# Kernel optimization log

Hardware: AMD Instinct MI355X
Metric: run time of the kernel (lower is better)

The kernel has to match this reference:

```python
import jax, jax.numpy as jnp
from jax import lax
import numpy as np

EPS = 1e-6
B, CIN, HW = 16, 12, 40
E, DEPTH, NH = 768, 12, 12
K, PAD = 10, 5
S = (HW + 2 * PAD - K) // 1 + 1  # 41 (series_len = s0); s1 also 41
L = S * S
HD = E // NH
MLP = 4 * E


def _ln(x, w, b):
    mu = x.mean(-1, keepdims=True)
    xc = x - mu
    var = (xc * xc).mean(-1, keepdims=True)
    return xc * lax.rsqrt(var + EPS) * w + b


def setup_inputs() -> dict:
    key = jax.random.key(0)
    ks = iter(jax.random.split(key, 24))
    r = lambda shape, s=0.02: jax.random.normal(next(ks), shape, jnp.float32) * s
    inp = {
        'x': jax.random.normal(next(ks), (B, CIN, HW, HW), jnp.float32),
        'conv_w': r((E, CIN, K, K)), 'conv_b': jnp.zeros((E,), jnp.float32),
        'pos_embed': r((1, L, E)),
        'ln1_w': jnp.ones((DEPTH, E), jnp.float32), 'ln1_b': jnp.zeros((DEPTH, E), jnp.float32),
        'qkv_w': r((DEPTH, E, 3 * E)), 'qkv_b': jnp.zeros((DEPTH, 3 * E), jnp.float32),
        'proj_w': r((DEPTH, E, E)), 'proj_b': jnp.zeros((DEPTH, E), jnp.float32),
        'ln2_w': jnp.ones((DEPTH, E), jnp.float32), 'ln2_b': jnp.zeros((DEPTH, E), jnp.float32),
        'fc1_w': r((DEPTH, E, MLP)), 'fc1_b': jnp.zeros((DEPTH, MLP), jnp.float32),
        'fc2_w': r((DEPTH, MLP, E)), 'fc2_b': jnp.zeros((DEPTH, E), jnp.float32),
        'lnf_w': jnp.ones((E,), jnp.float32), 'lnf_b': jnp.zeros((E,), jnp.float32),
        'tconv_w': r((E, 1, K, K)), 'tconv_b': jnp.zeros((1,), jnp.float32),
    }
    return inp


def reference(x, conv_w, conv_b, pos_embed, ln1_w, ln1_b, qkv_w, qkv_b,
              proj_w, proj_b, ln2_w, ln2_b, fc1_w, fc1_b, fc2_w, fc2_b,
              lnf_w, lnf_b, tconv_w, tconv_b):
    scale = HD ** -0.5
    # patch embed: Conv2d -> (B, E, 41, 41) -> flatten -> (B, L, E)
    h = lax.conv_general_dilated(x, conv_w, (1, 1), [(PAD, PAD), (PAD, PAD)])
    h = h + conv_b[None, :, None, None]
    t = h.reshape(B, E, L).transpose(0, 2, 1) + pos_embed

    for i in range(DEPTH):
        # attention over each of the S series slices (N = S tokens each), batched
        y = _ln(t, ln1_w[i], ln1_b[i])
        qkv = (y @ qkv_w[i] + qkv_b[i]).reshape(B, S, S, 3, NH, HD)
        q, k, v = qkv[:, :, :, 0], qkv[:, :, :, 1], qkv[:, :, :, 2]  # (B,S,N,NH,HD)
        attn = jnp.einsum('bsnhd,bsmhd->bshnm', q, k) * scale
        attn = jax.nn.softmax(attn, axis=-1)
        o = jnp.einsum('bshnm,bsmhd->bsnhd', attn, v).reshape(B, L, E)
        t = t + (o @ proj_w[i] + proj_b[i])
        # MLP
        z = _ln(t, ln2_w[i], ln2_b[i])
        z = jax.nn.gelu(z @ fc1_w[i] + fc1_b[i], approximate=False)
        t = t + (z @ fc2_w[i] + fc2_b[i])

    t = _ln(t, lnf_w, lnf_b)
    feat = t.reshape(B, S, S, E).transpose(0, 3, 1, 2)  # (B, E, 41, 41)
    # ConvTranspose2d(k=10, s=1, p=5) == direct conv with flipped/swapped kernel, pad k-1-p=4
    wt = jnp.flip(tconv_w, (2, 3)).transpose(1, 0, 2, 3)  # (out_c, E, K, K)
    out = lax.conv_general_dilated(feat, wt, (1, 1), [(K - 1 - PAD,) * 2] * 2)
    out = out + tconv_b[None, :, None, None]
    return jnp.squeeze(out)  # (B, 40, 40)
```

## Files before the change

kernel.cpp:

```cpp
#include <hip/hip_runtime.h>
#include <cstdint>

typedef __bf16 bf16_t;
typedef __attribute__((ext_vector_type(8))) __bf16 bf16x8;
typedef __attribute__((ext_vector_type(4))) __bf16 bf16x4;
typedef __attribute__((ext_vector_type(4))) float f32x4;

#define TOKENS 26896
#define LLEN   1681
#define SDIM   41
#define EDIM   768

__device__ __forceinline__ void gload_lds16(const bf16_t* g, bf16_t* l) {
  auto gp = reinterpret_cast<const __attribute__((address_space(1))) char*>(
      reinterpret_cast<uintptr_t>(g));
  auto lp = reinterpret_cast<__attribute__((address_space(3))) char*>(
      reinterpret_cast<uintptr_t>(l));
  __builtin_amdgcn_global_load_lds(gp, lp, 16, 0, 0);
}

enum { EPI_T_POS = 0, EPI_BF16 = 1, EPI_ADD_T = 2, EPI_GELU = 3, EPI_F32 = 4 };

template <int EPI>
__global__ __launch_bounds__(256, 3) void gemm4_kernel(
    const bf16_t* __restrict__ A, const bf16_t* __restrict__ Bt,
    const float* __restrict__ bias, float* __restrict__ fout,
    bf16_t* __restrict__ bout, const float* __restrict__ pos,
    int M, int N, int K, int ntn, int nwg, int mtiles)
{
  __shared__ bf16_t lds[3 * 8192];
  const int tid = threadIdx.x, wave = tid >> 6, lane = tid & 63;
  const int wr = wave >> 1, wc = wave & 1;

  int id = blockIdx.x;
  {
    const int q = nwg >> 3, r = nwg & 7;
    const int xcd = id & 7, ix = id >> 3;
    id = (xcd < r ? xcd * (q + 1) : r * (q + 1) + (xcd - r) * q) + ix;
  }
  const int gsz = mtiles * 6;
  const int cg  = id / gsz, rem = id % gsz;
  const int row0 = (rem / 6) * 128;
  const int col0 = (cg * 6 + rem % 6) * 128;
  const int NT = K >> 5;

  const int srow = tid >> 2;
  const int sswz = ((tid & 3) ^ ((srow >> 1) & 3)) * 8;
  const bf16_t* aptr[2];
  const bf16_t* bptr[2];
  #pragma unroll
  for (int p = 0; p < 2; ++p) {
    int ar = row0 + p * 64 + srow; if (ar > M - 1) ar = M - 1;
    int br = col0 + p * 64 + srow; if (br > N - 1) br = N - 1;
    aptr[p] = A  + (size_t)ar * K + sswz;
    bptr[p] = Bt + (size_t)br * K + sswz;
  }
  bf16_t* sdst = lds + tid * 8;

  #define STAGE(BUF, KT) do {                                   \
    const int koff_ = (KT) << 5;                                \
    gload_lds16(aptr[0] + koff_, sdst + (BUF)*8192);            \
    gload_lds16(aptr[1] + koff_, sdst + (BUF)*8192 + 2048);     \
    gload_lds16(bptr[0] + koff_, sdst + (BUF)*8192 + 4096);     \
    gload_lds16(bptr[1] + koff_, sdst + (BUF)*8192 + 6144);     \
  } while (0)

  const int l15 = lane & 15, l4 = lane >> 4;
  const int fswz = (l4 ^ ((l15 >> 1) & 3)) << 3;
  const bf16_t* lA = lds + (wr * 64 + l15) * 32 + fswz;
  const bf16_t* lB = lds + 4096 + (wc * 64 + l15) * 32 + fswz;

  f32x4 acc[4][4] = {};

  #define COMPUTE(BUF) do {                                     \
    bf16x8 fa[4], fb[4];                                        \
    _Pragma("unroll")                                           \
    for (int m_ = 0; m_ < 4; ++m_) fa[m_] = *(const bf16x8*)(lA + (BUF)*8192 + m_*512); \
    _Pragma("unroll")                                           \
    for (int n_ = 0; n_ < 4; ++n_) fb[n_] = *(const bf16x8*)(lB + (BUF)*8192 + n_*512); \
    _Pragma("unroll")                                           \
    for (int m_ = 0; m_ < 4; ++m_)                              \
      _Pragma("unroll")                                         \
      for (int n_ = 0; n_ < 4; ++n_)                            \
        acc[m_][n_] = __builtin_amdgcn_mfma_f32_16x16x32_bf16(fa[m_], fb[n_], acc[m_][n_], 0, 0, 0); \
  } while (0)

  #define STEP(SC, SN, T) do {                                  \
    if ((T) + 2 < NT) STAGE(SN, (T) + 2);                       \
    COMPUTE(SC);                                                \
    if ((T) + 2 < NT)      asm volatile("s_waitcnt vmcnt(4)" ::: "memory"); \
    else if ((T) + 1 < NT) asm volatile("s_waitcnt vmcnt(0)" ::: "memory"); \
    __builtin_amdgcn_s_barrier();                               \
    __builtin_amdgcn_sched_barrier(0);                          \
  } while (0)

  STAGE(0, 0);
  if (NT > 1) {
    STAGE(1, 1);
    asm volatile("s_waitcnt vmcnt(4)" ::: "memory");
  } else {
    asm volatile("s_waitcnt vmcnt(0)" ::: "memory");
  }
  __builtin_amdgcn_s_barrier();
  __builtin_amdgcn_sched_barrier(0);

  for (int kt = 0; kt < NT; kt += 3) {
    STEP(0, 2, kt);
    if (kt + 1 < NT) STEP(1, 0, kt + 1);
    if (kt + 2 < NT) STEP(2, 1, kt + 2);
  }
  #undef STEP
  #undef STAGE
  #undef COMPUTE

  const int rgrp = lane >> 4;
  #pragma unroll
  for (int m = 0; m < 4; ++m) {
    #pragma unroll
    for (int n = 0; n < 4; ++n) {
      const int col = col0 + wc * 64 + n * 16 + l15;
      if (col >= N) continue;
      const int rbase = row0 + wr * 64 + m * 16 + rgrp * 4;
      float bv = 0.f;
      if constexpr (EPI != EPI_F32) bv = bias[col];
      #pragma unroll
      for (int r = 0; r < 4; ++r) {
        const int rr = rbase + r;
        if (rr >= M) continue;
        const float v = acc[m][n][r] + bv;
        const size_t o = (size_t)rr * N + col;
        if constexpr (EPI == EPI_T_POS) {
          const int l = rr % LLEN;
          bout[o] = (bf16_t)(v + pos[(size_t)l * N + col]);
        } else if constexpr (EPI == EPI_BF16) {
          bout[o] = (bf16_t)v;
        } else if constexpr (EPI == EPI_ADD_T) {
          bout[o] = (bf16_t)((float)bout[o] + v);
        } else if constexpr (EPI == EPI_GELU) {
          const float u = v + 0.044715f * v * v * v;
          const float gg = v / (1.f + __expf(-1.5957691216f * u));
          bout[o] = (bf16_t)gg;
        } else {
          fout[o] = v;
        }
      }
    }
  }
}

__global__ __launch_bounds__(256) void gemm128_f32(
    const bf16_t* __restrict__ A, const bf16_t* __restrict__ Bt,
    float* __restrict__ fout, int M, int N, int K)
{
  __shared__ bf16_t As[128 * 32];
  __shared__ bf16_t Bs[128 * 32];
  const int tid = threadIdx.x, wave = tid >> 6, lane = tid & 63;
  const int row0 = blockIdx.x * 128, col0 = blockIdx.y * 128;
  const int wr = wave >> 1, wc = wave & 1;
  f32x4 acc[4][4] = {};
  const int srow = lane >> 2, skoff = (lane & 3) * 8;
  const int nsteps = K >> 5;
  for (int kt = 0; kt < nsteps; ++kt) {
    const int k0 = kt << 5;
    #pragma unroll
    for (int i = 0; i < 2; ++i) {
      const int r = (i * 4 + wave) * 16 + srow;
      int arow = row0 + r; if (arow > M - 1) arow = M - 1;
      int brow = col0 + r; if (brow > N - 1) brow = N - 1;
      gload_lds16(A  + (size_t)arow * K + k0 + skoff, &As[r * 32 + skoff]);
      gload_lds16(Bt + (size_t)brow * K + k0 + skoff, &Bs[r * 32 + skoff]);
    }
    asm volatile("s_waitcnt vmcnt(0)" ::: "memory");
    __syncthreads();
    const int lrow = lane & 15, lk = (lane >> 4) * 8;
    bf16x8 af[4], bfr[4];
    #pragma unroll
    for (int mi = 0; mi < 4; ++mi)
      af[mi] = *(const bf16x8*)&As[(wr * 64 + mi * 16 + lrow) * 32 + lk];
    #pragma unroll
    for (int ni = 0; ni < 4; ++ni)
      bfr[ni] = *(const bf16x8*)&Bs[(wc * 64 + ni * 16 + lrow) * 32 + lk];
    #pragma unroll
    for (int mi = 0; mi < 4; ++mi)
      #pragma unroll
      for (int ni = 0; ni < 4; ++ni)
        acc[mi][ni] = __builtin_amdgcn_mfma_f32_16x16x32_bf16(af[mi], bfr[ni], acc[mi][ni], 0, 0, 0);
    __syncthreads();
  }
  const int lcol = lane & 15, rgrp = lane >> 4;
  #pragma unroll
  for (int mi = 0; mi < 4; ++mi)
    #pragma unroll
    for (int ni = 0; ni < 4; ++ni) {
      const int col = col0 + wc * 64 + ni * 16 + lcol;
      if (col >= N) continue;
      const int rbase = row0 + wr * 64 + mi * 16 + rgrp * 4;
      #pragma unroll
      for (int r = 0; r < 4; ++r) {
        const int rr = rbase + r;
        if (rr >= M) continue;
        fout[(size_t)rr * N + col] = acc[mi][ni][r];
      }
    }
}

__global__ __launch_bounds__(256) void ln_kernel(
    const bf16_t* __restrict__ t, const float* __restrict__ w,
    const float* __restrict__ b, bf16_t* __restrict__ y)
{
  const int token = blockIdx.x * 4 + (threadIdx.x >> 6);
  const int lane  = threadIdx.x & 63;
  const bf16_t* xp = t + (size_t)token * EDIM;
  const bf16x8 a8 = *(const bf16x8*)(xp + lane * 8);
  const bf16x4 a4 = *(const bf16x4*)(xp + 512 + lane * 4);
  float va[12];
  #pragma unroll
  for (int j = 0; j < 8; ++j) va[j] = (float)a8[j];
  #pragma unroll
  for (int j = 0; j < 4; ++j) va[8 + j] = (float)a4[j];
  float s = 0.f;
  #pragma unroll
  for (int j = 0; j < 12; ++j) s += va[j];
  #pragma unroll
  for (int off = 32; off; off >>= 1) s += __shfl_xor(s, off);
  const float mu = s * (1.f / 768.f);
  float q = 0.f;
  #pragma unroll
  for (int j = 0; j < 12; ++j) { const float d = va[j] - mu; q += d * d; }
  #pragma unroll
  for (int off = 32; off; off >>= 1) q += __shfl_xor(q, off);
  const float rs = rsqrtf(q * (1.f / 768.f) + 1e-6f);

  bf16_t* yp = y + (size_t)token * EDIM;
  {
    const int e0 = lane * 8;
    const float4 w0 = ((const float4*)(w + e0))[0];
    const float4 w1 = ((const float4*)(w + e0))[1];
    const float4 b0 = ((const float4*)(b + e0))[0];
    const float4 b1 = ((const float4*)(b + e0))[1];
    bf16x8 o;
    o[0] = (bf16_t)((va[0] - mu) * rs * w0.x + b0.x);
    o[1] = (bf16_t)((va[1] - mu) * rs * w0.y + b0.y);
    o[2] = (bf16_t)((va[2] - mu) * rs * w0.z + b0.z);
    o[3] = (bf16_t)((va[3] - mu) * rs * w0.w + b0.w);
    o[4] = (bf16_t)((va[4] - mu) * rs * w1.x + b1.x);
    o[5] = (bf16_t)((va[5] - mu) * rs * w1.y + b1.y);
    o[6] = (bf16_t)((va[6] - mu) * rs * w1.z + b1.z);
    o[7] = (bf16_t)((va[7] - mu) * rs * w1.w + b1.w);
    *(bf16x8*)(yp + e0) = o;
  }
  {
    const int e0 = 512 + lane * 4;
    const float4 w0 = *(const float4*)(w + e0);
    const float4 b0 = *(const float4*)(b + e0);
    bf16x4 o;
    o[0] = (bf16_t)((va[8]  - mu) * rs * w0.x + b0.x);
    o[1] = (bf16_t)((va[9]  - mu) * rs * w0.y + b0.y);
    o[2] = (bf16_t)((va[10] - mu) * rs * w0.z + b0.z);
    o[3] = (bf16_t)((va[11] - mu) * rs * w0.w + b0.w);
    *(bf16x4*)(yp + e0) = o;
  }
}

__global__ __launch_bounds__(256) void attn_kernel(
    const bf16_t* __restrict__ qkv, bf16_t* __restrict__ o)
{
  const int blk = blockIdx.x;
  const int h  = blk % 12;
  const int bs = blk / 12;
  const int s1 = bs % SDIM;
  const int b  = bs / SDIM;
  __shared__ float Qs[SDIM][68], Ks[SDIM][68], Vs[SDIM][68], Ps[SDIM][44];
  const int tid = threadIdx.x;
  const size_t base = ((size_t)b * LLEN + (size_t)s1 * SDIM);

  for (int idx = tid; idx < SDIM * 8; idx += 256) {
    const int m = idx >> 3, c = idx & 7;
    const bf16_t* p = qkv + (base + m) * 2304 + h * 64 + c * 8;
    const bf16x8 qv = *(const bf16x8*)(p);
    const bf16x8 kv = *(const bf16x8*)(p + 768);
    const bf16x8 vv = *(const bf16x8*)(p + 1536);
    float4 f0, f1;
    f0.x = (float)qv[0]; f0.y = (float)qv[1]; f0.z = (float)qv[2]; f0.w = (float)qv[3];
    f1.x = (float)qv[4]; f1.y = (float)qv[5]; f1.z = (float)qv[6]; f1.w = (float)qv[7];
    *(float4*)&Qs[m][c * 8] = f0; *(float4*)&Qs[m][c * 8 + 4] = f1;
    f0.x = (float)kv[0]; f0.y = (float)kv[1]; f0.z = (float)kv[2]; f0.w = (float)kv[3];
    f1.x = (float)kv[4]; f1.y = (float)kv[5]; f1.z = (float)kv[6]; f1.w = (float)kv[7];
    *(float4*)&Ks[m][c * 8] = f0; *(float4*)&Ks[m][c * 8 + 4] = f1;
    f0.x = (float)vv[0]; f0.y = (float)vv[1]; f0.z = (float)vv[2]; f0.w = (float)vv[3];
    f1.x = (float)vv[4]; f1.y = (float)vv[5]; f1.z = (float)vv[6]; f1.w = (float)vv[7];
    *(float4*)&Vs[m][c * 8] = f0; *(float4*)&Vs[m][c * 8 + 4] = f1;
  }
  __syncthreads();

  for (int idx = tid; idx < SDIM * SDIM; idx += 256) {
    const int n = idx / SDIM, m = idx % SDIM;
    const float4* qn = (const float4*)&Qs[n][0];
    const float4* km = (const float4*)&Ks[m][0];
    float sx = 0.f, sy = 0.f, sz = 0.f, sw = 0.f;
    #pragma unroll
    for (int d4 = 0; d4 < 16; ++d4) {
      const float4 q = qn[d4], k = km[d4];
      sx += q.x * k.x; sy += q.y * k.y; sz += q.z * k.z; sw += q.w * k.w;
    }
    Ps[n][m] = (sx + sy + sz + sw) * 0.125f;
  }
  __syncthreads();

  {
    const int row = tid >> 2, sub = tid & 3;
    if (row < SDIM) {
      float mx = -1e30f;
      for (int m = sub; m < SDIM; m += 4) mx = fmaxf(mx, Ps[row][m]);
      mx = fmaxf(mx, __shfl_xor(mx, 1));
      mx = fmaxf(mx, __shfl_xor(mx, 2));
      float sum = 0.f;
      for (int m = sub; m < SDIM; m += 4) {
        const float e = __expf(Ps[row][m] - mx);
        Ps[row][m] = e;
        sum += e;
      }
      sum += __shfl_xor(sum, 1);
      sum += __shfl_xor(sum, 2);
      const float inv = 1.f / sum;
      for (int m = sub; m < SDIM; m += 4) Ps[row][m] *= inv;
    }
  }
  __syncthreads();

  for (int idx = tid; idx < SDIM * 16; idx += 256) {
    const int n = idx >> 4, dq = idx & 15;
    float ax = 0.f, ay = 0.f, az = 0.f, aw = 0.f;
    #pragma unroll
    for (int m = 0; m < SDIM; ++m) {
      const float pm = Ps[n][m];
      const float4 v = *(const float4*)&Vs[m][dq * 4];
      ax += pm * v.x; ay += pm * v.y; az += pm * v.z; aw += pm * v.w;
    }
    bf16x4 ov;
    ov[0] = (bf16_t)ax; ov[1] = (bf16_t)ay; ov[2] = (bf16_t)az; ov[3] = (bf16_t)aw;
    *(bf16x4*)(o + (base + n) * EDIM + h * 64 + dq * 4) = ov;
  }
}

__device__ __forceinline__ void tr_tile(
    const float* __restrict__ in, bf16_t* __restrict__ out,
    int K, int N, int tile, int tid)
{
  __shared__ float tls[32][33];
  const int ntn = N >> 5;
  const int k0 = (tile / ntn) * 32, n0 = (tile % ntn) * 32;
  const int tx = tid & 31, ty = tid >> 5;
  #pragma unroll
  for (int i = 0; i < 32; i += 8)
    tls[ty + i][tx] = in[(size_t)(k0 + ty + i) * N + n0 + tx];
  __syncthreads();
  #pragma unroll
  for (int i = 0; i < 32; i += 8)
    out[(size_t)(n0 + ty + i) * K + k0 + tx] = (bf16_t)tls[tx][ty + i];
}

__global__ __launch_bounds__(256) void transpose4_kernel(
    const float* __restrict__ qw, const float* __restrict__ pw,
    const float* __restrict__ f1, const float* __restrict__ f2,
    bf16_t* __restrict__ Wq, bf16_t* __restrict__ Wp,
    bf16_t* __restrict__ W1, bf16_t* __restrict__ W2)
{
  const int b = blockIdx.x, tid = threadIdx.x;
  if (b < 1728)       tr_tile(qw, Wq, 768, 2304, b, tid);
  else if (b < 2304)  tr_tile(pw, Wp, 768, 768, b - 1728, tid);
  else if (b < 4608)  tr_tile(f1, W1, 768, 3072, b - 2304, tid);
  else                tr_tile(f2, W2, 3072, 768, b - 4608, tid);
}

__global__ __launch_bounds__(256) void im2col_kernel(
    const float* __restrict__ x, bf16_t* __restrict__ col, int tok0, int ntok)
{
  const size_t idx = (size_t)blockIdx.x * 256 + threadIdx.x;
  if (idx >= (size_t)ntok * 1216) return;
  const int kk = (int)(idx % 1216);
  const size_t tok = tok0 + idx / 1216;
  const int b = (int)(tok / LLEN), l = (int)(tok % LLEN);
  const int s1 = l / SDIM, s2 = l % SDIM;
  float v = 0.f;
  if (kk < 1200) {
    const int cin = kk / 100, r = kk % 100, ky = r / 10, kx = r % 10;
    const int iy = s1 - 5 + ky, ix = s2 - 5 + kx;
    if (iy >= 0 && iy < 40 && ix >= 0 && ix < 40)
      v = x[((size_t)(b * 12 + cin) * 40 + iy) * 40 + ix];
  }
  col[idx] = (bf16_t)v;
}

__global__ __launch_bounds__(256) void convw_kernel(
    const float* __restrict__ w, bf16_t* __restrict__ out)
{
  const int idx = blockIdx.x * 256 + threadIdx.x;
  const int kk = idx % 1216, e = idx / 1216;
  const float v = (kk < 1200) ? w[(size_t)e * 1200 + kk] : 0.f;
  out[idx] = (bf16_t)v;
}

__global__ __launch_bounds__(256) void tconvw_kernel(
    const float* __restrict__ w, bf16_t* __restrict__ out)
{
  const int idx = blockIdx.x * 256 + threadIdx.x;
  const int e = idx % 768, tap = idx / 768;
  const int ky = tap / 10, kx = tap % 10;
  out[idx] = (bf16_t)w[(size_t)e * 100 + (9 - ky) * 10 + (9 - kx)];
}

__global__ __launch_bounds__(256) void outconv_kernel(
    const float* __restrict__ g, const float* __restrict__ tb,
    float* __restrict__ out)
{
  const int idx = blockIdx.x * 256 + threadIdx.x;
  if (idx >= 16 * 40 * 40) return;
  const int x = idx % 40, y = (idx / 40) % 40, b = idx / 1600;
  float s = tb[0];
  #pragma unroll
  for (int ky = 0; ky < 10; ++ky) {
    const int ty_ = y - 4 + ky;
    if (ty_ < 0 || ty_ >= SDIM) continue;
    #pragma unroll
    for (int kx = 0; kx < 10; ++kx) {
      const int tx_ = x - 4 + kx;
      if (tx_ < 0 || tx_ >= SDIM) continue;
      s += g[((size_t)b * LLEN + ty_ * SDIM + tx_) * 100 + ky * 10 + kx];
    }
  }
  out[idx] = s;
}

extern "C" void kernel_launch(void* const* d_in, const int* in_sizes, int n_in,
                              void* d_out, int out_size, void* d_ws, size_t ws_size,
                              hipStream_t stream)
{
  const float* x       = (const float*)d_in[0];
  const float* conv_w  = (const float*)d_in[1];
  const float* conv_b  = (const float*)d_in[2];
  const float* pos     = (const float*)d_in[3];
  const float* ln1_w   = (const float*)d_in[4];
  const float* ln1_b   = (const float*)d_in[5];
  const float* qkv_w   = (const float*)d_in[6];
  const float* qkv_b   = (const float*)d_in[7];
  const float* proj_w  = (const float*)d_in[8];
  const float* proj_b  = (const float*)d_in[9];
  const float* ln2_w   = (const float*)d_in[10];
  const float* ln2_b   = (const float*)d_in[11];
  const float* fc1_w   = (const float*)d_in[12];
  const float* fc1_b   = (const float*)d_in[13];
  const float* fc2_w   = (const float*)d_in[14];
  const float* fc2_b   = (const float*)d_in[15];
  const float* lnf_w   = (const float*)d_in[16];
  const float* lnf_b   = (const float*)d_in[17];
  const float* tconv_w = (const float*)d_in[18];
  const float* tconv_b = (const float*)d_in[19];
  float* out = (float*)d_out;

  const int nch = (ws_size >= 262200000UL) ? 1
                : (ws_size >= 179500000UL) ? 2 : 4;
  const int cht = TOKENS / nch;

  char* p = (char*)d_ws;
  auto alloc = [&](size_t bytes) {
    char* r = p;
    p += (bytes + 255) & ~(size_t)255;
    return r;
  };
  bf16_t* wbuf = (bf16_t*)alloc((size_t)768 * 9216 * 2);
  bf16_t* t    = (bf16_t*)alloc((size_t)TOKENS * EDIM * 2);
  bf16_t* ybuf = (bf16_t*)alloc((size_t)TOKENS * EDIM * 2);
  bf16_t* hbuf = (bf16_t*)alloc((size_t)cht * 3072 * 2);

  bf16_t* Wq = wbuf;
  bf16_t* Wp = Wq + (size_t)2304 * 768;
  bf16_t* W1 = Wp + (size_t)768 * 768;
  bf16_t* W2 = W1 + (size_t)3072 * 768;

  auto g4 = [&](int epi, const bf16_t* A, const bf16_t* Bt,
                const float* bias, bf16_t* bo, const float* pe,
                int M, int N, int K) {
    const int mtiles = (M + 127) / 128;
    const int ntn = N / 128;
    const int nwg = mtiles * ntn;
    switch (epi) {
      case EPI_T_POS: gemm4_kernel<EPI_T_POS><<<nwg, 256, 0, stream>>>(A, Bt, bias, nullptr, bo, pe, M, N, K, ntn, nwg, mtiles); break;
      case EPI_BF16:  gemm4_kernel<EPI_BF16 ><<<nwg, 256, 0, stream>>>(A, Bt, bias, nullptr, bo, pe, M, N, K, ntn, nwg, mtiles); break;
      case EPI_ADD_T: gemm4_kernel<EPI_ADD_T><<<nwg, 256, 0, stream>>>(A, Bt, bias, nullptr, bo, pe, M, N, K, ntn, nwg, mtiles); break;
      default:        gemm4_kernel<EPI_GELU ><<<nwg, 256, 0, stream>>>(A, Bt, bias, nullptr, bo, pe, M, N, K, ntn, nwg, mtiles); break;
    }
  };

  convw_kernel<<<(768 * 1216) / 256, 256, 0, stream>>>(conv_w, wbuf);
  for (int c = 0; c < nch; ++c) {
    const int tok0 = c * cht;
    im2col_kernel<<<(unsigned)(((size_t)cht * 1216 + 255) / 256), 256, 0, stream>>>(x, hbuf, tok0, cht);
    g4(EPI_T_POS, hbuf, wbuf, conv_b, t + (size_t)tok0 * EDIM, pos, cht, EDIM, 1216);
  }

  for (int i = 0; i < 12; ++i) {
    transpose4_kernel<<<6912, 256, 0, stream>>>(
        qkv_w + (size_t)i * 768 * 2304, proj_w + (size_t)i * 768 * 768,
        fc1_w + (size_t)i * 768 * 3072, fc2_w + (size_t)i * 3072 * 768,
        Wq, Wp, W1, W2);

    ln_kernel<<<TOKENS / 4, 256, 0, stream>>>(t, ln1_w + i * EDIM, ln1_b + i * EDIM, ybuf);
    for (int c = 0; c < nch; ++c) {
      const size_t ro = (size_t)c * cht;
      g4(EPI_BF16, ybuf + ro * EDIM, Wq, qkv_b + i * 2304, hbuf, nullptr, cht, 2304, 768);
      attn_kernel<<<(16 / nch) * SDIM * 12, 256, 0, stream>>>(hbuf, ybuf + ro * EDIM);
    }
    g4(EPI_ADD_T, ybuf, Wp, proj_b + i * EDIM, t, nullptr, TOKENS, EDIM, 768);

    ln_kernel<<<TOKENS / 4, 256, 0, stream>>>(t, ln2_w + i * EDIM, ln2_b + i * EDIM, ybuf);
    for (int c = 0; c < nch; ++c) {
      const size_t ro = (size_t)c * cht;
      g4(EPI_GELU, ybuf + ro * EDIM, W1, fc1_b + i * 3072, hbuf, nullptr, cht, 3072, 768);
      g4(EPI_ADD_T, hbuf, W2, fc2_b + i * EDIM, t + ro * EDIM, nullptr, cht, EDIM, 3072);
    }
  }

  ln_kernel<<<TOKENS / 4, 256, 0, stream>>>(t, lnf_w, lnf_b, ybuf);
  tconvw_kernel<<<(100 * 768) / 256, 256, 0, stream>>>(tconv_w, wbuf);
  gemm128_f32<<<dim3((TOKENS + 127) / 128, 1), 256, 0, stream>>>(ybuf, wbuf, (float*)hbuf, TOKENS, 100, 768);
  outconv_kernel<<<100, 256, 0, stream>>>((const float*)hbuf, tconv_b, out);
}
```

Before: 8.993 ms.

## Switch GEMM to double-buffered LDS pipeline and raise occupancy to 4 blocks

```diff
diff --git a/kernel.cpp b/kernel.cpp
--- a/kernel.cpp
+++ b/kernel.cpp
@@ -22,13 +22,13 @@
 enum { EPI_T_POS = 0, EPI_BF16 = 1, EPI_ADD_T = 2, EPI_GELU = 3, EPI_F32 = 4 };
 
 template <int EPI>
-__global__ __launch_bounds__(256, 3) void gemm4_kernel(
+__global__ __launch_bounds__(256, 4) void gemm4_kernel(
     const bf16_t* __restrict__ A, const bf16_t* __restrict__ Bt,
     const float* __restrict__ bias, float* __restrict__ fout,
     bf16_t* __restrict__ bout, const float* __restrict__ pos,
     int M, int N, int K, int ntn, int nwg, int mtiles)
 {
-  __shared__ bf16_t lds[3 * 8192];
+  __shared__ bf16_t lds[2 * 8192];
   const int tid = threadIdx.x, wave = tid >> 6, lane = tid & 63;
   const int wr = wave >> 1, wc = wave & 1;
 
@@ -85,31 +85,19 @@
         acc[m_][n_] = __builtin_amdgcn_mfma_f32_16x16x32_bf16(fa[m_], fb[n_], acc[m_][n_], 0, 0, 0); \
   } while (0)
 
-  #define STEP(SC, SN, T) do {                                  \
-    if ((T) + 2 < NT) STAGE(SN, (T) + 2);                       \
-    COMPUTE(SC);                                                \
-    if ((T) + 2 < NT)      asm volatile("s_waitcnt vmcnt(4)" ::: "memory"); \
-    else if ((T) + 1 < NT) asm volatile("s_waitcnt vmcnt(0)" ::: "memory"); \
-    __builtin_amdgcn_s_barrier();                               \
-    __builtin_amdgcn_sched_barrier(0);                          \
-  } while (0)
-
   STAGE(0, 0);
-  if (NT > 1) {
-    STAGE(1, 1);
-    asm volatile("s_waitcnt vmcnt(4)" ::: "memory");
-  } else {
-    asm volatile("s_waitcnt vmcnt(0)" ::: "memory");
-  }
-  __builtin_amdgcn_s_barrier();
-  __builtin_amdgcn_sched_barrier(0);
-
-  for (int kt = 0; kt < NT; kt += 3) {
-    STEP(0, 2, kt);
-    if (kt + 1 < NT) STEP(1, 0, kt + 1);
-    if (kt + 2 < NT) STEP(2, 1, kt + 2);
-  }
-  #undef STEP
+  __syncthreads();
+  int kt = 0;
+  while (kt + 2 <= NT) {
+    if (kt + 1 < NT) STAGE(1, kt + 1);
+    COMPUTE(0);
+    __syncthreads();
+    if (kt + 2 < NT) STAGE(0, kt + 2);
+    COMPUTE(1);
+    __syncthreads();
+    kt += 2;
+  }
+  if (kt < NT) COMPUTE(0);
   #undef STAGE
   #undef COMPUTE
 
```

Result: slower. 9.248 ms (+2.8%).
